# Kernel tuning notes

Hardware: AMD Instinct MI355X
Metric: run time of the kernel (lower is better)

## Reference

```python
import jax, jax.numpy as jnp
import numpy as np

N_IN = 128
N_H = 64
NEGSAMP_ROUND = 1


def setup_inputs() -> dict:
    key = jax.random.key(0)
    k1, k2, k3, k4 = jax.random.split(key, 4)
    B, S = 8192, 64
    seq1 = jax.random.normal(k1, (B, S, N_IN), dtype=jnp.float32)
    adj = jax.random.uniform(k2, (B, S, S), dtype=jnp.float32)
    # GCN linear (no bias) + separate bias param, xavier-uniform style init
    lim_fc = float(np.sqrt(6.0 / (N_IN + N_H)))
    W_fc = jax.random.uniform(k3, (N_H, N_IN), jnp.float32, -lim_fc, lim_fc)
    b_gcn = jnp.zeros((N_H,), jnp.float32)
    prelu_a = jnp.float32(0.25)  # torch PReLU default single param
    # Bilinear discriminator: weight [1, n_h, n_h], bias [1]
    lim_b = float(np.sqrt(6.0 / (N_H + N_H)))
    W_bil = jax.random.uniform(k4, (1, N_H, N_H), jnp.float32, -lim_b, lim_b)
    b_bil = jnp.zeros((1,), jnp.float32)
    return {"seq1": seq1, "adj": adj, "W_fc": W_fc, "b_gcn": b_gcn,
            "prelu_a": prelu_a, "W_bil": W_bil, "b_bil": b_bil}


def _bilinear(h, c, W_bil, b_bil):
    # nn.Bilinear(n_h, n_h, 1): out[b,o] = sum_ij h[b,i] W[o,i,j] c[b,j] + bias[o]
    return jnp.einsum('bi,oij,bj->bo', h, W_bil, c) + b_bil


def reference(seq1, adj, W_fc, b_gcn, prelu_a, W_bil, b_bil):
    # GCN: linear -> bmm with adjacency -> bias -> PReLU  (fused elementwise)
    seq_fts = jnp.einsum('bsi,hi->bsh', seq1, W_fc)          # [B,S,n_h]
    out = jnp.einsum('bst,bth->bsh', adj, seq_fts) + b_gcn   # [B,S,n_h]
    h_1 = jnp.where(out >= 0, out, prelu_a * out)            # PReLU
    # avg readout over context nodes; last node is the target
    c = jnp.mean(h_1[:, :-1, :], axis=1)                     # [B,n_h]
    h_mv = h_1[:, -1, :]                                     # [B,n_h]
    # Discriminator with batch-shift negative sampling
    scs = [_bilinear(h_mv, c, W_bil, b_bil)]
    c_mi = c
    for _ in range(NEGSAMP_ROUND):
        c_mi = jnp.concatenate([c_mi[-2:-1, :], c_mi[:-1, :]], axis=0)
        scs.append(_bilinear(h_mv, c_mi, W_bil, b_bil))
    logits = jnp.concatenate(scs, axis=0)                    # [(1+r)*B, 1]
    return logits, h_mv, c
```

## Files before the change

### kernel.cpp

```cpp
#include <hip/hip_runtime.h>
#include <hip/hip_bf16.h>

#define BB   8192
#define SS   64
#define NIN  128
#define NH   64
#define NB   8
#define GRID (BB / NB)

typedef __attribute__((ext_vector_type(8))) short  short8;
typedef __attribute__((ext_vector_type(4))) float  f32x4;

__device__ __forceinline__ unsigned short f2b(float f) {
    unsigned int u = __float_as_uint(f);
    u += 0x7FFF + ((u >> 16) & 1);
    return (unsigned short)(u >> 16);
}

__device__ __forceinline__ short8 cvt8(float4 x0, float4 x1) {
    short8 r;
    r[0] = (short)f2b(x0.x); r[1] = (short)f2b(x0.y);
    r[2] = (short)f2b(x0.z); r[3] = (short)f2b(x0.w);
    r[4] = (short)f2b(x1.x); r[5] = (short)f2b(x1.y);
    r[6] = (short)f2b(x1.z); r[7] = (short)f2b(x1.w);
    return r;
}

__global__ void conv_w(const float* __restrict__ wf, const float* __restrict__ wbil,
                       unsigned short* __restrict__ wsA, unsigned short* __restrict__ wsB) {
    int idx = blockIdx.x * blockDim.x + threadIdx.x;
    if (idx < NH * NIN) {
        int h = idx >> 7, i = idx & 127;
        int hj = h >> 4, m = h & 15, kk = i >> 5, g = (i >> 3) & 3, e = i & 7;
        wsA[(((hj * 4 + kk) * 64) + g * 16 + m) * 8 + e] = f2b(wf[idx]);
    } else if (idx < NH * NIN + NH * NH) {
        int q = idx - NH * NIN;
        int i = q >> 6, j = q & 63;
        int kk = i >> 5, g = (i >> 3) & 3, e = i & 7, nt = j >> 4, m = j & 15;
        wsB[(((kk * 4 + nt) * 64) + g * 16 + m) * 8 + e] = f2b(wbil[q]);
    }
}

__global__ __launch_bounds__(256, 4) void fused_gcn(
    const float* __restrict__ seq1, const float* __restrict__ adj,
    const unsigned short* __restrict__ wsA, const float* __restrict__ b_gcn,
    const float* __restrict__ prelu_a, float* __restrict__ out_hmv,
    float* __restrict__ out_c)
{
    __shared__ short8 Wlds[1024];
    __shared__ unsigned short ftsT[NH][72];
    __shared__ float c_part[4][NH];

    const int tid = threadIdx.x;
    const int w   = tid >> 6;
    const int l   = tid & 63;
    const int m   = l & 15;
    const int g   = l >> 4;
    const int bbase = blockIdx.x * NB;
    const int srow  = 16 * w + m;
    const int s0i   = 16 * w + 4 * g;

    {
        const uint4* src = reinterpret_cast<const uint4*>(wsA);
        uint4* dst = reinterpret_cast<uint4*>(Wlds);
        #pragma unroll
        for (int q = 0; q < 4; ++q) dst[tid + 256 * q] = src[tid + 256 * q];
    }

    const float pa = *prelu_a;
    float bg[4];
    #pragma unroll
    for (int hj = 0; hj < 4; ++hj) bg[hj] = b_gcn[16 * hj + m];

    float4 s0, s1, s2, s3, s4, s5, s6, s7;
    {
        const float4* sp = reinterpret_cast<const float4*>(seq1 + (size_t)bbase * (SS * NIN) + srow * NIN);
        s0 = sp[0 + 2 * g];  s1 = sp[1 + 2 * g];
        s2 = sp[8 + 2 * g];  s3 = sp[9 + 2 * g];
        s4 = sp[16 + 2 * g]; s5 = sp[17 + 2 * g];
        s6 = sp[24 + 2 * g]; s7 = sp[25 + 2 * g];
    }
    __syncthreads();

    #pragma unroll 1
    for (int j = 0; j < NB; ++j) {
        const int b = bbase + j;

        const float4* ap = reinterpret_cast<const float4*>(adj + (size_t)b * (SS * SS) + srow * SS);
        float4 a0 = ap[0 + 2 * g], a1 = ap[1 + 2 * g];
        float4 a2 = ap[8 + 2 * g], a3 = ap[9 + 2 * g];

        short8 af[4];
        af[0] = cvt8(s0, s1); af[1] = cvt8(s2, s3);
        af[2] = cvt8(s4, s5); af[3] = cvt8(s6, s7);

        if (j + 1 < NB) {
            const float4* sp = reinterpret_cast<const float4*>(seq1 + (size_t)(b + 1) * (SS * NIN) + srow * NIN);
            s0 = sp[0 + 2 * g];  s1 = sp[1 + 2 * g];
            s2 = sp[8 + 2 * g];  s3 = sp[9 + 2 * g];
            s4 = sp[16 + 2 * g]; s5 = sp[17 + 2 * g];
            s6 = sp[24 + 2 * g]; s7 = sp[25 + 2 * g];
        }

        f32x4 acc1[4];
        #pragma unroll
        for (int hj = 0; hj < 4; ++hj)
            for (int r = 0; r < 4; ++r) acc1[hj][r] = 0.f;
        #pragma unroll
        for (int hj = 0; hj < 4; ++hj) {
            #pragma unroll
            for (int kk = 0; kk < 4; ++kk) {
                short8 bf = Wlds[(hj * 4 + kk) * 64 + l];
                acc1[hj] = __builtin_amdgcn_mfma_f32_16x16x32_bf16(af[kk], bf, acc1[hj], 0, 0, 0);
            }
        }

        #pragma unroll
        for (int hj = 0; hj < 4; ++hj) {
            uint2 pk;
            pk.x = (unsigned)f2b(acc1[hj][0]) | ((unsigned)f2b(acc1[hj][1]) << 16);
            pk.y = (unsigned)f2b(acc1[hj][2]) | ((unsigned)f2b(acc1[hj][3]) << 16);
            *reinterpret_cast<uint2*>(&ftsT[16 * hj + m][s0i]) = pk;
        }

        short8 adf0 = cvt8(a0, a1);
        short8 adf1 = cvt8(a2, a3);

        asm volatile("s_waitcnt lgkmcnt(0)" ::: "memory");
        __builtin_amdgcn_s_barrier();
        asm volatile("" ::: "memory");

        f32x4 acc2[4];
        #pragma unroll
        for (int hj = 0; hj < 4; ++hj)
            for (int r = 0; r < 4; ++r) acc2[hj][r] = 0.f;
        #pragma unroll
        for (int hj = 0; hj < 4; ++hj) {
            short8 f0 = *reinterpret_cast<const short8*>(&ftsT[16 * hj + m][8 * g]);
            short8 f1 = *reinterpret_cast<const short8*>(&ftsT[16 * hj + m][8 * g + 32]);
            acc2[hj] = __builtin_amdgcn_mfma_f32_16x16x32_bf16(adf0, f0, acc2[hj], 0, 0, 0);
            acc2[hj] = __builtin_amdgcn_mfma_f32_16x16x32_bf16(adf1, f1, acc2[hj], 0, 0, 0);
        }

        #pragma unroll
        for (int hj = 0; hj < 4; ++hj) {
            const int h = 16 * hj + m;
            float part = 0.f;
            #pragma unroll
            for (int r = 0; r < 4; ++r) {
                float v = acc2[hj][r] + bg[hj];
                v = (v >= 0.f) ? v : pa * v;
                const int s = s0i + r;
                if (s < SS - 1) part += v;
                else            out_hmv[(size_t)b * NH + h] = v;
            }
            part += __shfl_xor(part, 16);
            part += __shfl_xor(part, 32);
            if (g == 0) c_part[w][h] = part;
        }

        asm volatile("s_waitcnt lgkmcnt(0)" ::: "memory");
        __builtin_amdgcn_s_barrier();
        asm volatile("" ::: "memory");

        if (tid < NH) {
            float tot = c_part[0][tid] + c_part[1][tid] + c_part[2][tid] + c_part[3][tid];
            out_c[(size_t)b * NH + tid] = tot * (1.0f / 63.0f);
        }
    }
}

__global__ __launch_bounds__(256) void bilinear_k(
    const float* __restrict__ hmv, const float* __restrict__ c,
    const unsigned short* __restrict__ wsB, const float* __restrict__ b_bil,
    float* __restrict__ logits)
{
    const int tid = threadIdx.x;
    const int w   = tid >> 6;
    const int l   = tid & 63;
    const int m   = l & 15;
    const int g   = l >> 4;
    const int bgrp = (blockIdx.x * 4 + w) * 16;

    const float4* hp = reinterpret_cast<const float4*>(hmv + (size_t)(bgrp + m) * NH);
    short8 af[2];
    af[0] = cvt8(hp[0 + 2 * g], hp[1 + 2 * g]);
    af[1] = cvt8(hp[8 + 2 * g], hp[9 + 2 * g]);

    const short8* wl = reinterpret_cast<const short8*>(wsB);
    f32x4 acc[4];
    #pragma unroll
    for (int nt = 0; nt < 4; ++nt)
        for (int r = 0; r < 4; ++r) acc[nt][r] = 0.f;
    #pragma unroll
    for (int kk = 0; kk < 2; ++kk) {
        #pragma unroll
        for (int nt = 0; nt < 4; ++nt) {
            short8 bf = wl[(kk * 4 + nt) * 64 + l];
            acc[nt] = __builtin_amdgcn_mfma_f32_16x16x32_bf16(af[kk], bf, acc[nt], 0, 0, 0);
        }
    }

    float t0[4] = {0.f, 0.f, 0.f, 0.f};
    float t1[4] = {0.f, 0.f, 0.f, 0.f};
    #pragma unroll
    for (int nt = 0; nt < 4; ++nt) {
        #pragma unroll
        for (int r = 0; r < 4; ++r) {
            const int bq = bgrp + 4 * g + r;
            const int bp = (bq == 0) ? (BB - 2) : (bq - 1);
            float cj = c[(size_t)bq * NH + 16 * nt + m];
            float cp = c[(size_t)bp * NH + 16 * nt + m];
            t0[r] = fmaf(acc[nt][r], cj, t0[r]);
            t1[r] = fmaf(acc[nt][r], cp, t1[r]);
        }
    }
    #pragma unroll
    for (int r = 0; r < 4; ++r) {
        #pragma unroll
        for (int off = 1; off < 16; off <<= 1) {
            t0[r] += __shfl_xor(t0[r], off);
            t1[r] += __shfl_xor(t1[r], off);
        }
    }
    if (m == 0) {
        const float bbv = b_bil[0];
        #pragma unroll
        for (int r = 0; r < 4; ++r) {
            const int bq = bgrp + 4 * g + r;
            logits[bq]      = t0[r] + bbv;
            logits[BB + bq] = t1[r] + bbv;
        }
    }
}

extern "C" void kernel_launch(void* const* d_in, const int* in_sizes, int n_in,
                              void* d_out, int out_size, void* d_ws, size_t ws_size,
                              hipStream_t stream) {
    const float* seq1    = (const float*)d_in[0];
    const float* adj     = (const float*)d_in[1];
    const float* W_fc    = (const float*)d_in[2];
    const float* b_gcn   = (const float*)d_in[3];
    const float* prelu_a = (const float*)d_in[4];
    const float* W_bil   = (const float*)d_in[5];
    const float* b_bil   = (const float*)d_in[6];

    float* out    = (float*)d_out;
    float* logits = out;
    float* hmv    = out + 2 * BB;
    float* cc     = hmv + (size_t)BB * NH;

    unsigned short* wsA = (unsigned short*)d_ws;
    unsigned short* wsB = wsA + NH * NIN;

    conv_w<<<(NH * NIN + NH * NH + 255) / 256, 256, 0, stream>>>(W_fc, W_bil, wsA, wsB);
    fused_gcn<<<GRID, 256, 0, stream>>>(seq1, adj, wsA, b_gcn, prelu_a, hmv, cc);
    bilinear_k<<<BB / 64, 256, 0, stream>>>(hmv, cc, wsB, b_bil, logits);
}
```

Measured before the change: 90.47 us.

## Double-buffer LDS to drop per-batch barrier, prefetch adj, convert W_fc in-kernel

Each block now converts W_fc to bf16 directly into LDS instead of copying a pre-packed buffer written by a separate conversion kernel. The adj tile for the next batch is prefetched during the current iteration. ftsT and c_part are double-buffered so the second barrier per iteration goes away, and the c reduction for batch j-1 is deferred to iteration j. The goal is less synchronisation and load latency per batch, at the cost of more LDS, more registers and redundant W_fc conversion in every block.

Result: no change. 91.51 us (+1.1%).

```diff
diff --git a/kernel.cpp b/kernel.cpp
--- a/kernel.cpp
+++ b/kernel.cpp
@@ -26,15 +26,9 @@
     return r;
 }
 
-__global__ void conv_w(const float* __restrict__ wf, const float* __restrict__ wbil,
-                       unsigned short* __restrict__ wsA, unsigned short* __restrict__ wsB) {
-    int idx = blockIdx.x * blockDim.x + threadIdx.x;
-    if (idx < NH * NIN) {
-        int h = idx >> 7, i = idx & 127;
-        int hj = h >> 4, m = h & 15, kk = i >> 5, g = (i >> 3) & 3, e = i & 7;
-        wsA[(((hj * 4 + kk) * 64) + g * 16 + m) * 8 + e] = f2b(wf[idx]);
-    } else if (idx < NH * NIN + NH * NH) {
-        int q = idx - NH * NIN;
+__global__ void conv_wbil(const float* __restrict__ wbil, unsigned short* __restrict__ wsB) {
+    int q = blockIdx.x * blockDim.x + threadIdx.x;
+    if (q < NH * NH) {
         int i = q >> 6, j = q & 63;
         int kk = i >> 5, g = (i >> 3) & 3, e = i & 7, nt = j >> 4, m = j & 15;
         wsB[(((kk * 4 + nt) * 64) + g * 16 + m) * 8 + e] = f2b(wbil[q]);
@@ -43,13 +37,13 @@
 
 __global__ __launch_bounds__(256, 4) void fused_gcn(
     const float* __restrict__ seq1, const float* __restrict__ adj,
-    const unsigned short* __restrict__ wsA, const float* __restrict__ b_gcn,
+    const float* __restrict__ W_fc, const float* __restrict__ b_gcn,
     const float* __restrict__ prelu_a, float* __restrict__ out_hmv,
     float* __restrict__ out_c)
 {
     __shared__ short8 Wlds[1024];
-    __shared__ unsigned short ftsT[NH][72];
-    __shared__ float c_part[4][NH];
+    __shared__ unsigned short ftsT[2][NH][72];
+    __shared__ float c_part[2][4][NH];
 
     const int tid = threadIdx.x;
     const int w   = tid >> 6;
@@ -60,35 +54,38 @@
     const int srow  = 16 * w + m;
     const int s0i   = 16 * w + 4 * g;
 
-    {
-        const uint4* src = reinterpret_cast<const uint4*>(wsA);
-        uint4* dst = reinterpret_cast<uint4*>(Wlds);
-        #pragma unroll
-        for (int q = 0; q < 4; ++q) dst[tid + 256 * q] = src[tid + 256 * q];
-    }
-
-    const float pa = *prelu_a;
-    float bg[4];
-    #pragma unroll
-    for (int hj = 0; hj < 4; ++hj) bg[hj] = b_gcn[16 * hj + m];
-
     float4 s0, s1, s2, s3, s4, s5, s6, s7;
+    float4 a0, a1, a2, a3;
     {
         const float4* sp = reinterpret_cast<const float4*>(seq1 + (size_t)bbase * (SS * NIN) + srow * NIN);
         s0 = sp[0 + 2 * g];  s1 = sp[1 + 2 * g];
         s2 = sp[8 + 2 * g];  s3 = sp[9 + 2 * g];
         s4 = sp[16 + 2 * g]; s5 = sp[17 + 2 * g];
         s6 = sp[24 + 2 * g]; s7 = sp[25 + 2 * g];
-    }
-    __syncthreads();
+        const float4* ap = reinterpret_cast<const float4*>(adj + (size_t)bbase * (SS * SS) + srow * SS);
+        a0 = ap[0 + 2 * g]; a1 = ap[1 + 2 * g];
+        a2 = ap[8 + 2 * g]; a3 = ap[9 + 2 * g];
+    }
+
+    #pragma unroll
+    for (int kk = 0; kk < 4; ++kk) {
+        const float4* wp = reinterpret_cast<const float4*>(W_fc + (16 * w + m) * NIN + 32 * kk + 8 * g);
+        Wlds[(w * 4 + kk) * 64 + l] = cvt8(wp[0], wp[1]);
+    }
+
+    const float pa = *prelu_a;
+    float bg[4];
+    #pragma unroll
+    for (int hj = 0; hj < 4; ++hj) bg[hj] = b_gcn[16 * hj + m];
+
+    asm volatile("s_waitcnt lgkmcnt(0)" ::: "memory");
+    __builtin_amdgcn_s_barrier();
+    asm volatile("" ::: "memory");
 
     #pragma unroll 1
     for (int j = 0; j < NB; ++j) {
         const int b = bbase + j;
-
-        const float4* ap = reinterpret_cast<const float4*>(adj + (size_t)b * (SS * SS) + srow * SS);
-        float4 a0 = ap[0 + 2 * g], a1 = ap[1 + 2 * g];
-        float4 a2 = ap[8 + 2 * g], a3 = ap[9 + 2 * g];
+        const int p = j & 1;
 
         short8 af[4];
         af[0] = cvt8(s0, s1); af[1] = cvt8(s2, s3);
@@ -115,16 +112,22 @@
             }
         }
 
+        short8 adf0 = cvt8(a0, a1);
+        short8 adf1 = cvt8(a2, a3);
+
+        if (j + 1 < NB) {
+            const float4* ap = reinterpret_cast<const float4*>(adj + (size_t)(b + 1) * (SS * SS) + srow * SS);
+            a0 = ap[0 + 2 * g]; a1 = ap[1 + 2 * g];
+            a2 = ap[8 + 2 * g]; a3 = ap[9 + 2 * g];
+        }
+
         #pragma unroll
         for (int hj = 0; hj < 4; ++hj) {
             uint2 pk;
             pk.x = (unsigned)f2b(acc1[hj][0]) | ((unsigned)f2b(acc1[hj][1]) << 16);
             pk.y = (unsigned)f2b(acc1[hj][2]) | ((unsigned)f2b(acc1[hj][3]) << 16);
-            *reinterpret_cast<uint2*>(&ftsT[16 * hj + m][s0i]) = pk;
-        }
-
-        short8 adf0 = cvt8(a0, a1);
-        short8 adf1 = cvt8(a2, a3);
+            *reinterpret_cast<uint2*>(&ftsT[p][16 * hj + m][s0i]) = pk;
+        }
 
         asm volatile("s_waitcnt lgkmcnt(0)" ::: "memory");
         __builtin_amdgcn_s_barrier();
@@ -136,8 +139,8 @@
             for (int r = 0; r < 4; ++r) acc2[hj][r] = 0.f;
         #pragma unroll
         for (int hj = 0; hj < 4; ++hj) {
-            short8 f0 = *reinterpret_cast<const short8*>(&ftsT[16 * hj + m][8 * g]);
-            short8 f1 = *reinterpret_cast<const short8*>(&ftsT[16 * hj + m][8 * g + 32]);
+            short8 f0 = *reinterpret_cast<const short8*>(&ftsT[p][16 * hj + m][8 * g]);
+            short8 f1 = *reinterpret_cast<const short8*>(&ftsT[p][16 * hj + m][8 * g + 32]);
             acc2[hj] = __builtin_amdgcn_mfma_f32_16x16x32_bf16(adf0, f0, acc2[hj], 0, 0, 0);
             acc2[hj] = __builtin_amdgcn_mfma_f32_16x16x32_bf16(adf1, f1, acc2[hj], 0, 0, 0);
         }
@@ -156,17 +159,23 @@
             }
             part += __shfl_xor(part, 16);
             part += __shfl_xor(part, 32);
-            if (g == 0) c_part[w][h] = part;
-        }
-
-        asm volatile("s_waitcnt lgkmcnt(0)" ::: "memory");
-        __builtin_amdgcn_s_barrier();
-        asm volatile("" ::: "memory");
-
-        if (tid < NH) {
-            float tot = c_part[0][tid] + c_part[1][tid] + c_part[2][tid] + c_part[3][tid];
-            out_c[(size_t)b * NH + tid] = tot * (1.0f / 63.0f);
-        }
+            if (g == 0) c_part[p][w][h] = part;
+        }
+
+        if (j > 0 && tid < NH) {
+            const int q = p ^ 1;
+            float tot = c_part[q][0][tid] + c_part[q][1][tid] + c_part[q][2][tid] + c_part[q][3][tid];
+            out_c[(size_t)(b - 1) * NH + tid] = tot * (1.0f / 63.0f);
+        }
+    }
+
+    asm volatile("s_waitcnt lgkmcnt(0)" ::: "memory");
+    __builtin_amdgcn_s_barrier();
+    asm volatile("" ::: "memory");
+    if (tid < NH) {
+        const int q = (NB - 1) & 1;
+        float tot = c_part[q][0][tid] + c_part[q][1][tid] + c_part[q][2][tid] + c_part[q][3][tid];
+        out_c[(size_t)(bbase + NB - 1) * NH + tid] = tot * (1.0f / 63.0f);
     }
 }
 
@@ -250,10 +259,9 @@
     float* hmv    = out + 2 * BB;
     float* cc     = hmv + (size_t)BB * NH;
 
-    unsigned short* wsA = (unsigned short*)d_ws;
-    unsigned short* wsB = wsA + NH * NIN;
-
-    conv_w<<<(NH * NIN + NH * NH + 255) / 256, 256, 0, stream>>>(W_fc, W_bil, wsA, wsB);
-    fused_gcn<<<GRID, 256, 0, stream>>>(seq1, adj, wsA, b_gcn, prelu_a, hmv, cc);
+    unsigned short* wsB = (unsigned short*)d_ws;
+
+    conv_wbil<<<(NH * NH + 255) / 256, 256, 0, stream>>>(W_bil, wsB);
+    fused_gcn<<<GRID, 256, 0, stream>>>(seq1, adj, W_fc, b_gcn, prelu_a, hmv, cc);
     bilinear_k<<<BB / 64, 256, 0, stream>>>(hmv, cc, wsB, b_bil, logits);
 }
```
